# Optimization experiments

Hardware: AMD Instinct MI355X
Metric: run time of the kernel (lower is better)

The kernel has to match this reference:

```python
import jax, jax.numpy as jnp
import numpy as np

B, S, D_IN, D_OUT = 4, 2048, 1024, 1024
N_TREES, DEPTH, N_HEADS = 12, 3, 3
N_INTERNAL = 2 ** DEPTH - 1  # 7
N_LEAVES = 2 ** DEPTH        # 8
TEMPERATURE = 1.0
SOFTPLUS_SHIFT = 0.5413      # softplus(0.5413) ~= 1.0, so init node temp ~ 1


def _build_path_indices(depth):
    """Root-to-leaf internal-node indices and go-left directions per leaf."""
    L = 2 ** depth
    pi = np.zeros((L, depth), np.int32)
    pd = np.zeros((L, depth), np.float32)
    for leaf in range(L):
        node = 0
        for d in range(depth):
            pi[leaf, d] = node
            bit = (leaf >> (depth - 1 - d)) & 1
            pd[leaf, d] = 1.0 - bit
            node = 2 * node + 1 + bit
    return pi, pd


def setup_inputs() -> dict:
    key = jax.random.key(0)
    ks = jax.random.split(key, 4)
    x = jax.random.normal(ks[0], (B, S, D_IN), dtype=jnp.float32)
    # normal(0, 0.1) routing init
    decision_weights = 0.1 * jax.random.normal(ks[1], (N_TREES, N_INTERNAL, D_IN), dtype=jnp.float32)
    decision_biases = jnp.zeros((N_TREES, N_INTERNAL), dtype=jnp.float32)
    node_temperature_logits = jnp.zeros((N_TREES, N_INTERNAL), dtype=jnp.float32)
    # nn.Linear default init ~ U(-1/sqrt(D), 1/sqrt(D)); use matching-scale normal
    gate_w = jax.random.normal(ks[2], (N_TREES, D_IN), dtype=jnp.float32) / np.sqrt(D_IN)
    gate_b = jnp.zeros((N_TREES,), dtype=jnp.float32)
    # xavier_normal over each [n_leaves, output_dim] slice
    xav_std = np.sqrt(2.0 / (N_LEAVES + D_OUT))
    leaf_outputs = xav_std * jax.random.normal(ks[3], (N_HEADS, N_TREES, N_LEAVES, D_OUT), dtype=jnp.float32)
    pi, pd = _build_path_indices(DEPTH)
    return {
        "x": x,
        "decision_weights": decision_weights,
        "decision_biases": decision_biases,
        "node_temperature_logits": node_temperature_logits,
        "gate_w": gate_w,
        "gate_b": gate_b,
        "leaf_outputs": leaf_outputs,
        "path_indices": jnp.asarray(pi),
        "path_dirs": jnp.asarray(pd),
    }


def reference(x, decision_weights, decision_biases, node_temperature_logits,
              gate_w, gate_b, leaf_outputs, path_indices, path_dirs):
    # decisions: [B, S, T, N_internal]
    decisions = jnp.einsum('bsd,tnd->bstn', x, decision_weights) + decision_biases
    node_temps = TEMPERATURE * jax.nn.softplus(node_temperature_logits + SOFTPLUS_SHIFT)
    decisions = jax.nn.sigmoid(decisions / node_temps)
    # gather nodes along each root->leaf path: [B, S, T, L, depth]
    relevant = decisions[..., path_indices]
    probs_per_level = path_dirs * relevant + (1.0 - path_dirs) * (1.0 - relevant)
    leaf_probs = probs_per_level.prod(axis=-1)  # [B, S, T, L]
    # softmax gate over trees: [B, S, T]
    weights = jax.nn.softmax(jnp.einsum('bsd,td->bst', x, gate_w) + gate_b, axis=-1)
    # fold tree gate into leaf probs, then contract leaves against leaf outputs
    routed = leaf_probs * weights[..., None]            # [B, S, T, L]
    out = jnp.einsum('bstl,htld->hbsd', routed, leaf_outputs)  # [H, B, S, Dout]
    return out
```

## Files before the change

### kernel.cpp

```cpp
#include <hip/hip_runtime.h>

typedef __attribute__((ext_vector_type(8))) short short8;
typedef __attribute__((ext_vector_type(4))) float floatx4;
typedef unsigned int uint;
typedef unsigned short ushort;
typedef __attribute__((ext_vector_type(4))) uint uintx4;

#define NTOK   8192
#define DIN    1024
#define DOUT   1024
#define NJ     96
#define TOKPB  32
#define XSTR   136
#define DSTR   97
#define SSTR   85
#define RSTR   104
#define LOT_H  (DOUT * NJ)

static __device__ inline ushort f2b(float f) {
    uint u = __builtin_bit_cast(uint, f);
    u = u + 0x7fffu + ((u >> 16) & 1u);
    return (ushort)(u >> 16);
}
static __device__ inline uint pack2(float a, float b) {
    return (uint)f2b(a) | ((uint)f2b(b) << 16);
}

__global__ __launch_bounds__(256) void k_prep(const float* __restrict__ lo,
                                              const float* __restrict__ dw,
                                              const float* __restrict__ gw,
                                              ushort* __restrict__ lot,
                                              ushort* __restrict__ wcat) {
    int i = blockIdx.x * 256 + threadIdx.x;
    if (i < 3 * LOT_H) {
        int h = i / LOT_H;
        int rem = i - h * LOT_H;
        int k = rem >> 10;
        int d = rem & 1023;
        lot[h * LOT_H + d * NJ + k] = f2b(lo[i]);
    } else {
        int j = i - 3 * LOT_H;
        int r = j >> 10, c = j & 1023;
        float v = (r < 84) ? dw[r * DIN + c] : gw[(r - 84) * DIN + c];
        wcat[j] = f2b(v);
    }
}

__global__ __launch_bounds__(256) void k_fused(
    const float* __restrict__ x,
    const ushort* __restrict__ wcat,
    const float* __restrict__ db,
    const float* __restrict__ ntl,
    const float* __restrict__ gb,
    const int*   __restrict__ pi,
    const float* __restrict__ pd,
    const ushort* __restrict__ lot,
    float* __restrict__ out)
{
    __shared__ __attribute__((aligned(16))) char smem[34816];
    __shared__ __attribute__((aligned(16))) ushort rt[TOKPB][RSTR];
    __shared__ float invt[84];
    __shared__ float biasf[96];
    __shared__ int   pis[24];
    __shared__ float pds[24];

    ushort* xl = (ushort*)smem;
    ushort* wl = (ushort*)(smem + TOKPB * XSTR * 2);
    float*  decis = (float*)smem;
    float*  sdecs = (float*)(smem + TOKPB * DSTR * 4);

    const int tid = threadIdx.x;
    const int tb  = blockIdx.x * TOKPB;

    if (tid < 84) {
        float z = ntl[tid] + 0.5413f;
        float sp = (z > 20.0f) ? z : log1pf(__expf(z));
        invt[tid]  = 1.0f / sp;
        biasf[tid] = db[tid];
    } else if (tid < 96) {
        biasf[tid] = gb[tid - 84];
    } else if (tid < 120) {
        pis[tid - 96] = pi[tid - 96];
    } else if (tid < 144) {
        pds[tid - 120] = pd[tid - 120];
    }

    const int wave = tid >> 6, lane = tid & 63;
    const int lrow = lane & 15, quad = lane >> 4;
    const int wm = wave & 1, wn = wave >> 1;

    floatx4 acc[3];
#pragma unroll
    for (int nt = 0; nt < 3; ++nt) acc[nt] = (floatx4)(0.0f);

    floatx4 xv[2][4];
    uintx4  wv[2][6];

#define LOADX(B, KC) do { \
    _Pragma("unroll") for (int i_ = 0; i_ < 4; ++i_) { \
        int idx_ = tid + 256 * i_; \
        int r_ = idx_ >> 5, c_ = idx_ & 31; \
        xv[B][i_] = __builtin_nontemporal_load( \
            (const floatx4*)(x + (size_t)(tb + r_) * DIN + (KC) * 128 + c_ * 4)); \
    } } while (0)

#define LOADW(B, KC) do { \
    _Pragma("unroll") for (int i_ = 0; i_ < 6; ++i_) { \
        int idx_ = tid + 256 * i_; \
        int r_ = idx_ >> 4, c_ = idx_ & 15; \
        wv[B][i_] = *(const uintx4*)(wcat + r_ * DIN + (KC) * 128 + c_ * 8); \
    } } while (0)

#define STAGE(B) do { \
    _Pragma("unroll") for (int i_ = 0; i_ < 4; ++i_) { \
        int idx_ = tid + 256 * i_; \
        int r_ = idx_ >> 5, c_ = idx_ & 31; \
        uint2 p_; \
        p_.x = pack2(xv[B][i_][0], xv[B][i_][1]); \
        p_.y = pack2(xv[B][i_][2], xv[B][i_][3]); \
        *(uint2*)(xl + r_ * XSTR + c_ * 4) = p_; \
    } \
    _Pragma("unroll") for (int i_ = 0; i_ < 6; ++i_) { \
        int idx_ = tid + 256 * i_; \
        int r_ = idx_ >> 4, c_ = idx_ & 15; \
        *(uintx4*)(wl + r_ * XSTR + c_ * 8) = wv[B][i_]; \
    } } while (0)

    LOADX(0, 0);
    LOADW(0, 0);

#pragma unroll
    for (int kc = 0; kc < 8; ++kc) {
        const int cur = kc & 1, nxt = cur ^ 1;
        __syncthreads();
        STAGE(cur);
        __syncthreads();
        if (kc < 7) {
            LOADX(nxt, kc + 1);
            LOADW(nxt, kc + 1);
        }

        short8 a[4];
#pragma unroll
        for (int kt = 0; kt < 4; ++kt)
            a[kt] = *(const short8*)(xl + (wm * 16 + lrow) * XSTR + kt * 32 + quad * 8);
#pragma unroll
        for (int nt = 0; nt < 3; ++nt) {
#pragma unroll
            for (int kt = 0; kt < 4; ++kt) {
                short8 b = *(const short8*)(wl + (wn * 48 + nt * 16 + lrow) * XSTR + kt * 32 + quad * 8);
                acc[nt] = __builtin_amdgcn_mfma_f32_16x16x32_bf16(a[kt], b, acc[nt], 0, 0, 0);
            }
        }
    }
#undef LOADX
#undef LOADW
#undef STAGE

    __syncthreads();
#pragma unroll
    for (int nt = 0; nt < 3; ++nt)
#pragma unroll
        for (int r = 0; r < 4; ++r)
            decis[(wm * 16 + quad * 4 + r) * DSTR + wn * 48 + nt * 16 + lrow] = acc[nt][r];
    __syncthreads();

#pragma unroll
    for (int i = 0; i < 11; ++i) {
        int idx = tid + 256 * i;
        if (idx < TOKPB * 84) {
            int tk = idx / 84, nd = idx - tk * 84;
            float dv = (decis[tk * DSTR + nd] + biasf[nd]) * invt[nd];
            sdecs[tk * SSTR + nd] = 1.0f / (1.0f + __expf(-dv));
        }
    }
    __syncthreads();

    {
        const int tk = tid >> 3, l = tid & 7;
        float g[12], gm = -1e30f;
#pragma unroll
        for (int tt = 0; tt < 12; ++tt) {
            g[tt] = decis[tk * DSTR + 84 + tt] + biasf[84 + tt];
            gm = fmaxf(gm, g[tt]);
        }
        float gs = 0.0f;
#pragma unroll
        for (int tt = 0; tt < 12; ++tt) { g[tt] = __expf(g[tt] - gm); gs += g[tt]; }
        float ginv = 1.0f / gs;

        const int   n0 = pis[l * 3 + 0], n1 = pis[l * 3 + 1], n2 = pis[l * 3 + 2];
        const float d0 = pds[l * 3 + 0], d1 = pds[l * 3 + 1], d2 = pds[l * 3 + 2];
        const float* sd = sdecs + tk * SSTR;
#pragma unroll
        for (int t = 0; t < 12; ++t) {
            float s0 = sd[t * 7 + n0], s1 = sd[t * 7 + n1], s2 = sd[t * 7 + n2];
            float pb = g[t] * ginv
                     * (d0 * s0 + (1.0f - d0) * (1.0f - s0))
                     * (d1 * s1 + (1.0f - d1) * (1.0f - s1))
                     * (d2 * s2 + (1.0f - d2) * (1.0f - s2));
            rt[tk][t * 8 + l] = f2b(pb);
        }
    }
    __syncthreads();

    {
        short8 a0[3], a1[3];
#pragma unroll
        for (int kk = 0; kk < 3; ++kk) {
            a0[kk] = *(const short8*)(&rt[lrow][quad * 8 + kk * 32]);
            a1[kk] = *(const short8*)(&rt[16 + lrow][quad * 8 + kk * 32]);
        }
#pragma unroll 4
        for (int nt = 0; nt < 48; ++nt) {
            int c = wave * 768 + nt * 16;
            int h = c >> 10;
            int d = (c & 1023) + lrow;
            const ushort* bp = lot + (size_t)h * LOT_H + (size_t)d * NJ + quad * 8;
            floatx4 c0 = (floatx4)(0.0f), c1 = (floatx4)(0.0f);
#pragma unroll
            for (int kk = 0; kk < 3; ++kk) {
                short8 b = *(const short8*)(bp + kk * 32);
                c0 = __builtin_amdgcn_mfma_f32_16x16x32_bf16(a0[kk], b, c0, 0, 0, 0);
                c1 = __builtin_amdgcn_mfma_f32_16x16x32_bf16(a1[kk], b, c1, 0, 0, 0);
            }
            float* ob = out + ((size_t)h * NTOK + tb) * DOUT + d;
#pragma unroll
            for (int r = 0; r < 4; ++r) {
                __builtin_nontemporal_store(c0[r], ob + (size_t)(quad * 4 + r) * DOUT);
                __builtin_nontemporal_store(c1[r], ob + (size_t)(16 + quad * 4 + r) * DOUT);
            }
        }
    }
}

extern "C" void kernel_launch(void* const* d_in, const int* in_sizes, int n_in,
                              void* d_out, int out_size, void* d_ws, size_t ws_size,
                              hipStream_t stream) {
    const float* x   = (const float*)d_in[0];
    const float* dw  = (const float*)d_in[1];
    const float* db  = (const float*)d_in[2];
    const float* ntl = (const float*)d_in[3];
    const float* gw  = (const float*)d_in[4];
    const float* gb  = (const float*)d_in[5];
    const float* lo  = (const float*)d_in[6];
    const int*   pi  = (const int*)d_in[7];
    const float* pd  = (const float*)d_in[8];
    float* out = (float*)d_out;

    ushort* lot  = (ushort*)d_ws;
    ushort* wcat = lot + (size_t)3 * LOT_H;

    k_prep<<<dim3((3 * LOT_H + NJ * DIN) / 256), dim3(256), 0, stream>>>(lo, dw, gw, lot, wcat);
    k_fused<<<dim3(NTOK / TOKPB), dim3(256), 0, stream>>>(x, wcat, db, ntl, gb, pi, pd, lot, out);
}
```

Before: 161.1 us.

## Halve tokens per block and software-pipeline leaf-output loads in the output GEMM

Tokens per block drop from 32 to 16, which doubles the grid to 512 blocks, and launch bounds now request two blocks per CU. The routing GEMM's wave-to-tile mapping is reworked so each wave covers one or two 16-column tiles. The output stage now double-buffers the leaf-output B fragments in registers, loading the next group of four tiles while the MFMAs run on the current group. This aims at better latency hiding and occupancy, but each block re-reads the full weight and leaf tables for half as many tokens, so L2 traffic per token roughly doubles.

Result: no change. 162.7 us (+1.0%).

```diff
diff --git a/kernel.cpp b/kernel.cpp
--- a/kernel.cpp
+++ b/kernel.cpp
@@ -10,7 +10,7 @@
 #define DIN    1024
 #define DOUT   1024
 #define NJ     96
-#define TOKPB  32
+#define TOKPB  16
 #define XSTR   136
 #define DSTR   97
 #define SSTR   85
@@ -46,7 +46,7 @@
     }
 }
 
-__global__ __launch_bounds__(256) void k_fused(
+__global__ __launch_bounds__(256, 2) void k_fused(
     const float* __restrict__ x,
     const ushort* __restrict__ wcat,
     const float* __restrict__ db,
@@ -57,7 +57,7 @@
     const ushort* __restrict__ lot,
     float* __restrict__ out)
 {
-    __shared__ __attribute__((aligned(16))) char smem[34816];
+    __shared__ __attribute__((aligned(16))) char smem[30464];
     __shared__ __attribute__((aligned(16))) ushort rt[TOKPB][RSTR];
     __shared__ float invt[84];
     __shared__ float biasf[96];
@@ -87,17 +87,18 @@
 
     const int wave = tid >> 6, lane = tid & 63;
     const int lrow = lane & 15, quad = lane >> 4;
-    const int wm = wave & 1, wn = wave >> 1;
-
-    floatx4 acc[3];
-#pragma unroll
-    for (int nt = 0; nt < 3; ++nt) acc[nt] = (floatx4)(0.0f);
-
-    floatx4 xv[2][4];
+
+    const int nt0 = wave;
+    const bool two = (wave < 2);
+    const int nt1 = wave + 4;
+
+    floatx4 acc0 = (floatx4)(0.0f), acc1 = (floatx4)(0.0f);
+
+    floatx4 xv[2][2];
     uintx4  wv[2][6];
 
 #define LOADX(B, KC) do { \
-    _Pragma("unroll") for (int i_ = 0; i_ < 4; ++i_) { \
+    _Pragma("unroll") for (int i_ = 0; i_ < 2; ++i_) { \
         int idx_ = tid + 256 * i_; \
         int r_ = idx_ >> 5, c_ = idx_ & 31; \
         xv[B][i_] = __builtin_nontemporal_load( \
@@ -112,7 +113,7 @@
     } } while (0)
 
 #define STAGE(B) do { \
-    _Pragma("unroll") for (int i_ = 0; i_ < 4; ++i_) { \
+    _Pragma("unroll") for (int i_ = 0; i_ < 2; ++i_) { \
         int idx_ = tid + 256 * i_; \
         int r_ = idx_ >> 5, c_ = idx_ & 31; \
         uint2 p_; \
@@ -143,13 +144,17 @@
         short8 a[4];
 #pragma unroll
         for (int kt = 0; kt < 4; ++kt)
-            a[kt] = *(const short8*)(xl + (wm * 16 + lrow) * XSTR + kt * 32 + quad * 8);
-#pragma unroll
-        for (int nt = 0; nt < 3; ++nt) {
+            a[kt] = *(const short8*)(xl + lrow * XSTR + kt * 32 + quad * 8);
+#pragma unroll
+        for (int kt = 0; kt < 4; ++kt) {
+            short8 b0 = *(const short8*)(wl + (nt0 * 16 + lrow) * XSTR + kt * 32 + quad * 8);
+            acc0 = __builtin_amdgcn_mfma_f32_16x16x32_bf16(a[kt], b0, acc0, 0, 0, 0);
+        }
+        if (two) {
 #pragma unroll
             for (int kt = 0; kt < 4; ++kt) {
-                short8 b = *(const short8*)(wl + (wn * 48 + nt * 16 + lrow) * XSTR + kt * 32 + quad * 8);
-                acc[nt] = __builtin_amdgcn_mfma_f32_16x16x32_bf16(a[kt], b, acc[nt], 0, 0, 0);
+                short8 b1 = *(const short8*)(wl + (nt1 * 16 + lrow) * XSTR + kt * 32 + quad * 8);
+                acc1 = __builtin_amdgcn_mfma_f32_16x16x32_bf16(a[kt], b1, acc1, 0, 0, 0);
             }
         }
     }
@@ -159,14 +164,17 @@
 
     __syncthreads();
 #pragma unroll
-    for (int nt = 0; nt < 3; ++nt)
+    for (int r = 0; r < 4; ++r)
+        decis[(quad * 4 + r) * DSTR + nt0 * 16 + lrow] = acc0[r];
+    if (two) {
 #pragma unroll
         for (int r = 0; r < 4; ++r)
-            decis[(wm * 16 + quad * 4 + r) * DSTR + wn * 48 + nt * 16 + lrow] = acc[nt][r];
-    __syncthreads();
-
-#pragma unroll
-    for (int i = 0; i < 11; ++i) {
+            decis[(quad * 4 + r) * DSTR + nt1 * 16 + lrow] = acc1[r];
+    }
+    __syncthreads();
+
+#pragma unroll
+    for (int i = 0; i < 6; ++i) {
         int idx = tid + 256 * i;
         if (idx < TOKPB * 84) {
             int tk = idx / 84, nd = idx - tk * 84;
@@ -177,7 +185,7 @@
     __syncthreads();
 
     {
-        const int tk = tid >> 3, l = tid & 7;
+        const int tk = tid >> 4, l = (tid >> 1) & 7, th = tid & 1;
         float g[12], gm = -1e30f;
 #pragma unroll
         for (int tt = 0; tt < 12; ++tt) {
@@ -192,45 +200,58 @@
         const int   n0 = pis[l * 3 + 0], n1 = pis[l * 3 + 1], n2 = pis[l * 3 + 2];
         const float d0 = pds[l * 3 + 0], d1 = pds[l * 3 + 1], d2 = pds[l * 3 + 2];
         const float* sd = sdecs + tk * SSTR;
-#pragma unroll
-        for (int t = 0; t < 12; ++t) {
-            float s0 = sd[t * 7 + n0], s1 = sd[t * 7 + n1], s2 = sd[t * 7 + n2];
-            float pb = g[t] * ginv
+        const int t0 = th * 6;
+#pragma unroll
+        for (int t = 0; t < 6; ++t) {
+            int tt = t0 + t;
+            float s0 = sd[tt * 7 + n0], s1 = sd[tt * 7 + n1], s2 = sd[tt * 7 + n2];
+            float pb = g[tt] * ginv
                      * (d0 * s0 + (1.0f - d0) * (1.0f - s0))
                      * (d1 * s1 + (1.0f - d1) * (1.0f - s1))
                      * (d2 * s2 + (1.0f - d2) * (1.0f - s2));
-            rt[tk][t * 8 + l] = f2b(pb);
+            rt[tk][tt * 8 + l] = f2b(pb);
         }
     }
     __syncthreads();
 
     {
-        short8 a0[3], a1[3];
-#pragma unroll
-        for (int kk = 0; kk < 3; ++kk) {
-            a0[kk] = *(const short8*)(&rt[lrow][quad * 8 + kk * 32]);
-            a1[kk] = *(const short8*)(&rt[16 + lrow][quad * 8 + kk * 32]);
-        }
-#pragma unroll 4
-        for (int nt = 0; nt < 48; ++nt) {
-            int c = wave * 768 + nt * 16;
-            int h = c >> 10;
-            int d = (c & 1023) + lrow;
-            const ushort* bp = lot + (size_t)h * LOT_H + (size_t)d * NJ + quad * 8;
-            floatx4 c0 = (floatx4)(0.0f), c1 = (floatx4)(0.0f);
-#pragma unroll
-            for (int kk = 0; kk < 3; ++kk) {
-                short8 b = *(const short8*)(bp + kk * 32);
-                c0 = __builtin_amdgcn_mfma_f32_16x16x32_bf16(a0[kk], b, c0, 0, 0, 0);
-                c1 = __builtin_amdgcn_mfma_f32_16x16x32_bf16(a1[kk], b, c1, 0, 0, 0);
+        short8 a[3];
+#pragma unroll
+        for (int kk = 0; kk < 3; ++kk)
+            a[kk] = *(const short8*)(&rt[lrow][quad * 8 + kk * 32]);
+
+        short8 bb[2][12];
+#define LOADB(B, G) do { \
+    _Pragma("unroll") for (int q_ = 0; q_ < 4; ++q_) { \
+        int c_ = wave * 768 + ((G) * 4 + q_) * 16; \
+        int h_ = c_ >> 10; \
+        int d_ = (c_ & 1023) + lrow; \
+        const ushort* bp_ = lot + (size_t)h_ * LOT_H + (size_t)d_ * NJ + quad * 8; \
+        _Pragma("unroll") for (int kk_ = 0; kk_ < 3; ++kk_) \
+            bb[B][q_ * 3 + kk_] = *(const short8*)(bp_ + kk_ * 32); \
+    } } while (0)
+
+        LOADB(0, 0);
+#pragma unroll
+        for (int g = 0; g < 12; ++g) {
+            const int cur = g & 1;
+            if (g < 11) LOADB(cur ^ 1, g + 1);
+#pragma unroll
+            for (int q = 0; q < 4; ++q) {
+                floatx4 c0 = (floatx4)(0.0f);
+#pragma unroll
+                for (int kk = 0; kk < 3; ++kk)
+                    c0 = __builtin_amdgcn_mfma_f32_16x16x32_bf16(a[kk], bb[cur][q * 3 + kk], c0, 0, 0, 0);
+                int c = wave * 768 + (g * 4 + q) * 16;
+                int h = c >> 10;
+                int d = (c & 1023) + lrow;
+                float* ob = out + ((size_t)h * NTOK + tb) * DOUT + d;
+#pragma unroll
+                for (int r = 0; r < 4; ++r)
+                    __builtin_nontemporal_store(c0[r], ob + (size_t)(quad * 4 + r) * DOUT);
             }
-            float* ob = out + ((size_t)h * NTOK + tb) * DOUT + d;
-#pragma unroll
-            for (int r = 0; r < 4; ++r) {
-                __builtin_nontemporal_store(c0[r], ob + (size_t)(quad * 4 + r) * DOUT);
-                __builtin_nontemporal_store(c1[r], ob + (size_t)(16 + quad * 4 + r) * DOUT);
-            }
-        }
+        }
+#undef LOADB
     }
 }
 
```
